# Kernel tuning notes

Hardware: AMD Instinct MI355X
Metric: run time of the kernel (lower is better)

Reference implementation:

```python
import jax, jax.numpy as jnp
import numpy as np

N, F, H, L, O, E = 20000, 128, 128, 4, 64, 640000
NEG_SLOPE = 0.2  # PyG GATConv default


def setup_inputs() -> dict:
    key = jax.random.key(0)
    ks = jax.random.split(key, 8)
    x = jax.random.normal(ks[0], (N, F), dtype=jnp.float32)
    edge_index = jax.random.randint(ks[1], (2, E), 0, N, dtype=jnp.int64)
    sc = 1.0 / np.sqrt(F)
    Ws = jax.random.normal(ks[2], (L, F, H), dtype=jnp.float32) * sc
    att_src = jax.random.normal(ks[3], (L, H), dtype=jnp.float32) * sc
    att_dst = jax.random.normal(ks[4], (L, H), dtype=jnp.float32) * sc
    biases = jnp.zeros((L, H), dtype=jnp.float32)
    W_out = jax.random.normal(ks[5], (H, O), dtype=jnp.float32) * (1.0 / np.sqrt(H))
    b_out = jnp.zeros((O,), dtype=jnp.float32)
    return {"x": x, "edge_index": edge_index, "Ws": Ws, "att_src": att_src,
            "att_dst": att_dst, "biases": biases, "W_out": W_out, "b_out": b_out}


def _gat_conv(h, src, dst, W, a_s, a_d, b):
    # h: [N, F_in]; single-head GATConv (PyG semantics)
    z = h @ W                                   # [N, H]
    alpha_s = z @ a_s                           # [N]
    alpha_d = z @ a_d                           # [N]
    logits = jax.nn.leaky_relu(alpha_s[src] + alpha_d[dst], negative_slope=NEG_SLOPE)  # [E']
    # segment-softmax over edges grouped by destination node
    m = jax.ops.segment_max(logits, dst, num_segments=N)
    p = jnp.exp(logits - m[dst])
    s = jax.ops.segment_sum(p, dst, num_segments=N)
    alpha = p / (s[dst] + 1e-16)                # [E']
    out = jax.ops.segment_sum(alpha[:, None] * z[src], dst, num_segments=N)  # [N, H]
    return out + b


def reference(x, edge_index, Ws, att_src, att_dst, biases, W_out, b_out):
    # add self-loops once (PyG GATConv default add_self_loops=True)
    loop = jnp.arange(N, dtype=edge_index.dtype)
    src = jnp.concatenate([edge_index[0], loop])
    dst = jnp.concatenate([edge_index[1], loop])
    h = x
    for l in range(L):
        h = _gat_conv(h, src, dst, Ws[l], att_src[l], att_dst[l], biases[l])
        h = jax.nn.relu(h)  # Dropout is identity at eval
    return h @ W_out + b_out  # [N, O]
```

## Files before the change

### kernel.cpp

```cpp
#include <hip/hip_runtime.h>

#define NN 20000
#define FF 128
#define HH 128
#define LL 4
#define OO 64
#define EE 640000
#define ET (EE + NN)
#define NEG 0.2f
#define NB ((NN + 255) / 256)
#define NTILES (NN / 16)

typedef short bf16x8 __attribute__((ext_vector_type(8)));
typedef float f32x4 __attribute__((ext_vector_type(4)));

__device__ inline ushort f2bf(float f) {
    uint u = __float_as_uint(f);
    return (ushort)((u + 0x7fffu + ((u >> 16) & 1u)) >> 16);
}


__global__ void k_init_counters(int* __restrict__ counters) {
    int i = blockIdx.x * 256 + threadIdx.x;
    if (i < NN) counters[i] = 1;
}

__global__ void k_hist(const int* __restrict__ dst, int* __restrict__ counters) {
    int e = blockIdx.x * 256 + threadIdx.x;
    if (e < EE) atomicAdd(&counters[dst[e]], 1);
}

__global__ void k_partial(const int* __restrict__ counters, int* __restrict__ partials) {
    __shared__ int ws[4];
    int t = threadIdx.x;
    int i = blockIdx.x * 256 + t;
    int c = (i < NN) ? counters[i] : 0;
    #pragma unroll
    for (int off = 32; off; off >>= 1) c += __shfl_xor(c, off);
    if ((t & 63) == 0) ws[t >> 6] = c;
    __syncthreads();
    if (t == 0) partials[blockIdx.x] = ws[0] + ws[1] + ws[2] + ws[3];
}

__global__ void k_scan_small(const int* __restrict__ partials, int* __restrict__ offsets) {
    __shared__ int sp[128];
    int t = threadIdx.x;
    int v = (t < NB) ? partials[t] : 0;
    sp[t] = v;
    __syncthreads();
    for (int off = 1; off < 128; off <<= 1) {
        int u = (t >= off) ? sp[t - off] : 0;
        __syncthreads();
        sp[t] += u;
        __syncthreads();
    }
    if (t < NB) offsets[t] = sp[t] - v;
}

__global__ void k_apply(const int* __restrict__ counters, const int* __restrict__ offsets,
                        int* __restrict__ row_off, int* __restrict__ cursor,
                        int2* __restrict__ edges) {
    __shared__ int sc[256];
    int t = threadIdx.x;
    int i = blockIdx.x * 256 + t;
    int c = (i < NN) ? counters[i] : 0;
    sc[t] = c;
    __syncthreads();
    for (int off = 1; off < 256; off <<= 1) {
        int u = (t >= off) ? sc[t - off] : 0;
        __syncthreads();
        sc[t] += u;
        __syncthreads();
    }
    int incl = sc[t];
    int base = offsets[blockIdx.x];
    if (i < NN) {
        int excl = base + incl - c;
        row_off[i] = excl;
        cursor[i] = excl + 1;
        edges[excl] = make_int2(i, i);
        if (i == NN - 1) row_off[NN] = base + incl;
    }
}

__global__ void k_scatter(const int* __restrict__ src, const int* __restrict__ dst,
                          int* __restrict__ cursor, int2* __restrict__ edges) {
    int e = blockIdx.x * 256 + threadIdx.x;
    if (e < EE) {
        int d = dst[e];
        int pidx = atomicAdd(&cursor[d], 1);
        edges[pidx] = make_int2(src[e], d);
    }
}


__global__ void k_convw(const float* __restrict__ Ws, const float* __restrict__ Wout,
                        ushort* __restrict__ wh, ushort* __restrict__ wl) {
    int idx = blockIdx.x * 256 + threadIdx.x;
    const int per_l = HH * 128;
    float v;
    if (idx < LL * per_l) {
        int l = idx / per_l, rem = idx % per_l;
        int n = rem >> 7, k = rem & 127;
        v = Ws[(size_t)l * 128 * HH + (size_t)k * HH + n];
    } else {
        int j = idx - LL * per_l;
        if (j >= OO * 128) return;
        int n = j >> 7, k = j & 127;
        v = Wout[(size_t)k * OO + n];
    }
    ushort h = f2bf(v);
    float hf = __uint_as_float((uint)h << 16);
    wh[idx] = h;
    wl[idx] = f2bf(v - hf);
}


__global__ void k_wa(const float* __restrict__ Ws, const float* __restrict__ attS,
                     const float* __restrict__ attD, float* __restrict__ wa) {
    int t = blockIdx.x * 256 + threadIdx.x;
    if (t >= LL * 256) return;
    int l = t >> 8, rem = t & 255, which = rem >> 7, k = rem & 127;
    const float* wrow = Ws + (size_t)l * 128 * HH + (size_t)k * HH;
    const float* av = (which ? attD : attS) + l * HH;
    float s = 0.f;
    #pragma unroll 4
    for (int n = 0; n < HH; n++) s += wrow[n] * av[n];
    wa[l * 256 + which * 128 + k] = s;
}


__global__ void k_ew(const float* __restrict__ asv, const float* __restrict__ adv,
                     const int2* __restrict__ edges, float2* __restrict__ pe) {
    int e = blockIdx.x * 256 + threadIdx.x;
    if (e >= ET) return;
    int2 ed = edges[e];
    float ad_ = adv[ed.y];
    float ls = asv[ed.x] + ad_;  ls = (ls >= 0.f) ? ls : NEG * ls;
    float ld = asv[ed.y] + ad_;  ld = (ld >= 0.f) ? ld : NEG * ld;
    float2 o;
    o.x = __expf(ls - ld);
    o.y = __int_as_float(ed.x);
    pe[e] = o;
}


__global__ __launch_bounds__(256)
void k_agg(const float* __restrict__ z, const float2* __restrict__ pe,
           const int* __restrict__ row_off, const float* __restrict__ bias,
           float* __restrict__ h) {
    int node = blockIdx.x * 4 + (threadIdx.x >> 6);
    int l64 = threadIdx.x & 63;
    if (node >= NN) return;
    int g = l64 >> 5, cl = l64 & 31;
    int beg = row_off[node], end = row_off[node + 1], lim = end - 1;
    const float4* zb = (const float4*)z;

    float4 acc = make_float4(0.f, 0.f, 0.f, 0.f);
    float s = 0.f;
    for (int e = beg + g * 8; e < end; e += 16) {
        int i1 = min(e + 1, lim), i2 = min(e + 2, lim), i3 = min(e + 3, lim);
        int i4 = min(e + 4, lim), i5 = min(e + 5, lim), i6 = min(e + 6, lim), i7 = min(e + 7, lim);
        float2 q0 = pe[e],  q1 = pe[i1], q2 = pe[i2], q3 = pe[i3];
        float2 q4 = pe[i4], q5 = pe[i5], q6 = pe[i6], q7 = pe[i7];
        int s0 = __float_as_int(q0.y), s1 = __float_as_int(q1.y);
        int s2 = __float_as_int(q2.y), s3 = __float_as_int(q3.y);
        int s4 = __float_as_int(q4.y), s5 = __float_as_int(q5.y);
        int s6 = __float_as_int(q6.y), s7 = __float_as_int(q7.y);
        float p0 = q0.x;
        float p1 = (e + 1 < end) ? q1.x : 0.f;
        float p2 = (e + 2 < end) ? q2.x : 0.f;
        float p3 = (e + 3 < end) ? q3.x : 0.f;
        float p4 = (e + 4 < end) ? q4.x : 0.f;
        float p5 = (e + 5 < end) ? q5.x : 0.f;
        float p6 = (e + 6 < end) ? q6.x : 0.f;
        float p7 = (e + 7 < end) ? q7.x : 0.f;
        float4 z0 = zb[(size_t)s0 * 32 + cl];
        float4 z1 = zb[(size_t)s1 * 32 + cl];
        float4 z2 = zb[(size_t)s2 * 32 + cl];
        float4 z3 = zb[(size_t)s3 * 32 + cl];
        float4 z4 = zb[(size_t)s4 * 32 + cl];
        float4 z5 = zb[(size_t)s5 * 32 + cl];
        float4 z6 = zb[(size_t)s6 * 32 + cl];
        float4 z7 = zb[(size_t)s7 * 32 + cl];
        s += ((p0 + p1) + (p2 + p3)) + ((p4 + p5) + (p6 + p7));
        acc.x += (p0 * z0.x + p1 * z1.x + p2 * z2.x + p3 * z3.x)
               + (p4 * z4.x + p5 * z5.x + p6 * z6.x + p7 * z7.x);
        acc.y += (p0 * z0.y + p1 * z1.y + p2 * z2.y + p3 * z3.y)
               + (p4 * z4.y + p5 * z5.y + p6 * z6.y + p7 * z7.y);
        acc.z += (p0 * z0.z + p1 * z1.z + p2 * z2.z + p3 * z3.z)
               + (p4 * z4.z + p5 * z5.z + p6 * z6.z + p7 * z7.z);
        acc.w += (p0 * z0.w + p1 * z1.w + p2 * z2.w + p3 * z3.w)
               + (p4 * z4.w + p5 * z5.w + p6 * z6.w + p7 * z7.w);
    }

    acc.x += __shfl_xor(acc.x, 32);
    acc.y += __shfl_xor(acc.y, 32);
    acc.z += __shfl_xor(acc.z, 32);
    acc.w += __shfl_xor(acc.w, 32);
    s     += __shfl_xor(s, 32);

    if (g == 0) {
        float inv = 1.f / (s + 1e-16f);
        float4 b = ((const float4*)bias)[cl];
        float4 o;
        o.x = fmaxf(acc.x * inv + b.x, 0.f);
        o.y = fmaxf(acc.y * inv + b.y, 0.f);
        o.z = fmaxf(acc.z * inv + b.z, 0.f);
        o.w = fmaxf(acc.w * inv + b.w, 0.f);
        ((float4*)h)[(size_t)node * 32 + cl] = o;
    }
}


template <int NCOL, bool BIAS, bool ALPHAS>
__global__ __launch_bounds__(256)
void k_gemm2(const float* __restrict__ A, const ushort* __restrict__ wh,
             const ushort* __restrict__ wl, const float* __restrict__ bias,
             float* __restrict__ C, const float* __restrict__ wa,
             float* __restrict__ as_o, float* __restrict__ ad_o) {
    __shared__ float h[16][132];
    int t = threadIdx.x;
    int row0 = blockIdx.x * 16;
    for (int i = t; i < 512; i += 256) {
        int r = i >> 5, c4 = (i & 31) << 2;
        *(float4*)&h[r][c4] = *(const float4*)&A[(size_t)(row0 + r) * 128 + c4];
    }
    __syncthreads();

    int wid = t >> 6, l64 = t & 63;
    constexpr int CT = NCOL / 32;
    if (wid >= CT) return;
    int lr = l64 & 15, lg = l64 >> 4;
    int col0 = wid * 32;

    f32x4 af0[4], af1[4];
    #pragma unroll
    for (int s = 0; s < 4; s++) {
        af0[s] = *(const f32x4*)&h[lr][s * 32 + lg * 8];
        af1[s] = *(const f32x4*)&h[lr][s * 32 + lg * 8 + 4];
    }
    bf16x8 ah[4], al[4];
    #pragma unroll
    for (int s = 0; s < 4; s++) {
        #pragma unroll
        for (int j = 0; j < 8; j++) {
            float v = (j < 4) ? af0[s][j] : af1[s][j - 4];
            ushort hb = f2bf(v);
            float hf = __uint_as_float((uint)hb << 16);
            ah[s][j] = (short)hb;
            al[s][j] = (short)f2bf(v - hf);
        }
    }

    f32x4 acc[2] = {{0.f, 0.f, 0.f, 0.f}, {0.f, 0.f, 0.f, 0.f}};
    #pragma unroll
    for (int s = 0; s < 4; s++) {
        #pragma unroll
        for (int nt = 0; nt < 2; nt++) {
            int woff = (col0 + nt * 16 + lr) * 128 + s * 32 + lg * 8;
            bf16x8 bh = *(const bf16x8*)(wh + woff);
            bf16x8 bl = *(const bf16x8*)(wl + woff);
            acc[nt] = __builtin_amdgcn_mfma_f32_16x16x32_bf16(ah[s], bh, acc[nt], 0, 0, 0);
            acc[nt] = __builtin_amdgcn_mfma_f32_16x16x32_bf16(ah[s], bl, acc[nt], 0, 0, 0);
            acc[nt] = __builtin_amdgcn_mfma_f32_16x16x32_bf16(al[s], bh, acc[nt], 0, 0, 0);
        }
    }

    int orow = lg * 4;
    #pragma unroll
    for (int nt = 0; nt < 2; nt++) {
        int c = col0 + nt * 16 + lr;
        #pragma unroll
        for (int r = 0; r < 4; r++) {
            float v = acc[nt][r];
            if (BIAS) v += bias[c];
            C[(size_t)(row0 + orow + r) * NCOL + c] = v;
        }
    }

    if constexpr (ALPHAS) {
        if (wid == 0) {
            float ps = 0.f, pd = 0.f;
            #pragma unroll
            for (int s = 0; s < 4; s++) {
                #pragma unroll
                for (int j = 0; j < 8; j++) {
                    float v = (j < 4) ? af0[s][j] : af1[s][j - 4];
                    int k = s * 32 + lg * 8 + j;
                    ps += v * wa[k];
                    pd += v * wa[128 + k];
                }
            }
            ps += __shfl_xor(ps, 16);  pd += __shfl_xor(pd, 16);
            ps += __shfl_xor(ps, 32);  pd += __shfl_xor(pd, 32);
            if (lg == 0) {
                as_o[row0 + lr] = ps;
                ad_o[row0 + lr] = pd;
            }
        }
    }
}


extern "C" void kernel_launch(void* const* d_in, const int* in_sizes, int n_in,
                              void* d_out, int out_size, void* d_ws, size_t ws_size,
                              hipStream_t stream) {
    const float* x      = (const float*)d_in[0];
    const int*   ei     = (const int*)d_in[1];
    const float* Ws     = (const float*)d_in[2];
    const float* attS   = (const float*)d_in[3];
    const float* attD   = (const float*)d_in[4];
    const float* biases = (const float*)d_in[5];
    const float* W_out  = (const float*)d_in[6];
    const float* b_out  = (const float*)d_in[7];
    float* out = (float*)d_out;

    const int* srcp = ei;
    const int* dstp = ei + EE;

    char* w = (char*)d_ws;
    auto take = [&](size_t bytes) {
        char* p = w;
        w += (bytes + 15) & ~(size_t)15;
        return p;
    };
    float*  za         = (float*)take((size_t)NN * HH * 4);
    float*  zbv        = (float*)take((size_t)NN * HH * 4);
    float*  hbuf       = (float*)take((size_t)NN * HH * 4);
    float*  asa        = (float*)take((size_t)NN * 4);
    float*  ada        = (float*)take((size_t)NN * 4);
    float*  asb        = (float*)take((size_t)NN * 4);
    float*  adb        = (float*)take((size_t)NN * 4);
    int*    counters   = (int*)take((size_t)NN * 4);
    int*    row_off    = (int*)take((size_t)(NN + 1) * 4);
    int*    cursor     = (int*)take((size_t)NN * 4);
    int2*   edges      = (int2*)take((size_t)ET * 8);
    float2* pebuf      = (float2*)take((size_t)ET * 8);
    int*    partials   = (int*)take((size_t)NB * 4);
    int*    offsets    = (int*)take((size_t)NB * 4);
    const int WTOT = LL * HH * 128 + OO * 128;
    ushort* whbuf      = (ushort*)take((size_t)WTOT * 2);
    ushort* wlbuf      = (ushort*)take((size_t)WTOT * 2);
    float*  wabuf      = (float*)take((size_t)LL * 256 * 4);

    k_init_counters<<<(NN + 255) / 256, 256, 0, stream>>>(counters);
    k_hist<<<(EE + 255) / 256, 256, 0, stream>>>(dstp, counters);
    k_partial<<<NB, 256, 0, stream>>>(counters, partials);
    k_scan_small<<<1, 128, 0, stream>>>(partials, offsets);
    k_apply<<<NB, 256, 0, stream>>>(counters, offsets, row_off, cursor, edges);
    k_scatter<<<(EE + 255) / 256, 256, 0, stream>>>(srcp, dstp, cursor, edges);
    k_convw<<<(WTOT + 255) / 256, 256, 0, stream>>>(Ws, W_out, whbuf, wlbuf);
    k_wa<<<(LL * 256 + 255) / 256, 256, 0, stream>>>(Ws, attS, attD, wabuf);

    const int agg_blocks = (NN + 3) / 4;
    const int ew_blocks  = (ET + 255) / 256;

    k_gemm2<HH, false, true><<<NTILES, 256, 0, stream>>>(
        x, whbuf, wlbuf, nullptr, za, wabuf, asa, ada);

    const float* zi[3]  = {za, zbv, za};
    float*       zo[3]  = {zbv, za, zbv};
    const float* asi[3] = {asa, asb, asa};
    const float* adi[3] = {ada, adb, ada};
    float*       aso[3] = {asb, asa, asb};
    float*       ado[3] = {adb, ada, adb};
    for (int l = 0; l < 3; l++) {
        k_ew<<<ew_blocks, 256, 0, stream>>>(asi[l], adi[l], edges, pebuf);
        k_agg<<<agg_blocks, 256, 0, stream>>>(zi[l], pebuf, row_off,
                                              biases + l * HH, hbuf);
        k_gemm2<HH, false, true><<<NTILES, 256, 0, stream>>>(
            hbuf, whbuf + (size_t)(l + 1) * HH * 128, wlbuf + (size_t)(l + 1) * HH * 128,
            nullptr, zo[l], wabuf + (l + 1) * 256, aso[l], ado[l]);
    }

    k_ew<<<ew_blocks, 256, 0, stream>>>(asb, adb, edges, pebuf);
    k_agg<<<agg_blocks, 256, 0, stream>>>(zbv, pebuf, row_off,
                                          biases + 3 * HH, hbuf);
    k_gemm2<OO, true, false><<<NTILES, 256, 0, stream>>>(
        hbuf, whbuf + (size_t)LL * HH * 128, wlbuf + (size_t)LL * HH * 128,
        b_out, out, nullptr, nullptr, nullptr);
}
```

Baseline: 321.6 us.

## Split aggregation into four column-slab passes over a slab-packed z layout

The GEMM now writes z in a packed layout of four 32-column slabs, each contiguous over all nodes ([4][N][32]). Aggregation becomes four launches, one per slab, with 8 lanes per edge covering 32 columns and 8 edges in flight per wave. The aim is to keep each pass's gathered working set (about 2.5 MB per slab) resident in cache so random source-row gathers hit L2 instead of HBM. The cost is reading the CSR and edge-weight arrays four times, four times as many launches, and fewer independent gathers per lane.

```diff
diff --git a/kernel.cpp b/kernel.cpp
--- a/kernel.cpp
+++ b/kernel.cpp
@@ -146,74 +146,56 @@
 
 
 __global__ __launch_bounds__(256)
-void k_agg(const float* __restrict__ z, const float2* __restrict__ pe,
-           const int* __restrict__ row_off, const float* __restrict__ bias,
-           float* __restrict__ h) {
+void k_aggq(const float* __restrict__ zq, const float2* __restrict__ pe,
+            const int* __restrict__ row_off, const float* __restrict__ bias,
+            float* __restrict__ h, int q) {
     int node = blockIdx.x * 4 + (threadIdx.x >> 6);
     int l64 = threadIdx.x & 63;
     if (node >= NN) return;
-    int g = l64 >> 5, cl = l64 & 31;
+    int c4 = l64 & 7, ep = l64 >> 3;
     int beg = row_off[node], end = row_off[node + 1], lim = end - 1;
-    const float4* zb = (const float4*)z;
+    const float* qb = zq + (size_t)q * NN * 32;
 
     float4 acc = make_float4(0.f, 0.f, 0.f, 0.f);
     float s = 0.f;
-    for (int e = beg + g * 8; e < end; e += 16) {
-        int i1 = min(e + 1, lim), i2 = min(e + 2, lim), i3 = min(e + 3, lim);
-        int i4 = min(e + 4, lim), i5 = min(e + 5, lim), i6 = min(e + 6, lim), i7 = min(e + 7, lim);
-        float2 q0 = pe[e],  q1 = pe[i1], q2 = pe[i2], q3 = pe[i3];
-        float2 q4 = pe[i4], q5 = pe[i5], q6 = pe[i6], q7 = pe[i7];
+    for (int e = beg + ep; e < end; e += 16) {
+        int i1 = min(e + 8, lim);
+        float2 q0 = pe[e], q1 = pe[i1];
         int s0 = __float_as_int(q0.y), s1 = __float_as_int(q1.y);
-        int s2 = __float_as_int(q2.y), s3 = __float_as_int(q3.y);
-        int s4 = __float_as_int(q4.y), s5 = __float_as_int(q5.y);
-        int s6 = __float_as_int(q6.y), s7 = __float_as_int(q7.y);
         float p0 = q0.x;
-        float p1 = (e + 1 < end) ? q1.x : 0.f;
-        float p2 = (e + 2 < end) ? q2.x : 0.f;
-        float p3 = (e + 3 < end) ? q3.x : 0.f;
-        float p4 = (e + 4 < end) ? q4.x : 0.f;
-        float p5 = (e + 5 < end) ? q5.x : 0.f;
-        float p6 = (e + 6 < end) ? q6.x : 0.f;
-        float p7 = (e + 7 < end) ? q7.x : 0.f;
-        float4 z0 = zb[(size_t)s0 * 32 + cl];
-        float4 z1 = zb[(size_t)s1 * 32 + cl];
-        float4 z2 = zb[(size_t)s2 * 32 + cl];
-        float4 z3 = zb[(size_t)s3 * 32 + cl];
-        float4 z4 = zb[(size_t)s4 * 32 + cl];
-        float4 z5 = zb[(size_t)s5 * 32 + cl];
-        float4 z6 = zb[(size_t)s6 * 32 + cl];
-        float4 z7 = zb[(size_t)s7 * 32 + cl];
-        s += ((p0 + p1) + (p2 + p3)) + ((p4 + p5) + (p6 + p7));
-        acc.x += (p0 * z0.x + p1 * z1.x + p2 * z2.x + p3 * z3.x)
-               + (p4 * z4.x + p5 * z5.x + p6 * z6.x + p7 * z7.x);
-        acc.y += (p0 * z0.y + p1 * z1.y + p2 * z2.y + p3 * z3.y)
-               + (p4 * z4.y + p5 * z5.y + p6 * z6.y + p7 * z7.y);
-        acc.z += (p0 * z0.z + p1 * z1.z + p2 * z2.z + p3 * z3.z)
-               + (p4 * z4.z + p5 * z5.z + p6 * z6.z + p7 * z7.z);
-        acc.w += (p0 * z0.w + p1 * z1.w + p2 * z2.w + p3 * z3.w)
-               + (p4 * z4.w + p5 * z5.w + p6 * z6.w + p7 * z7.w);
-    }
-
-    acc.x += __shfl_xor(acc.x, 32);
-    acc.y += __shfl_xor(acc.y, 32);
-    acc.z += __shfl_xor(acc.z, 32);
-    acc.w += __shfl_xor(acc.w, 32);
-    s     += __shfl_xor(s, 32);
-
-    if (g == 0) {
+        float p1 = (e + 8 < end) ? q1.x : 0.f;
+        float4 z0 = *(const float4*)(qb + (size_t)s0 * 32 + c4 * 4);
+        float4 z1 = *(const float4*)(qb + (size_t)s1 * 32 + c4 * 4);
+        s += p0 + p1;
+        acc.x += p0 * z0.x + p1 * z1.x;
+        acc.y += p0 * z0.y + p1 * z1.y;
+        acc.z += p0 * z0.z + p1 * z1.z;
+        acc.w += p0 * z0.w + p1 * z1.w;
+    }
+
+    #pragma unroll
+    for (int off = 8; off < 64; off <<= 1) {
+        acc.x += __shfl_xor(acc.x, off);
+        acc.y += __shfl_xor(acc.y, off);
+        acc.z += __shfl_xor(acc.z, off);
+        acc.w += __shfl_xor(acc.w, off);
+        s     += __shfl_xor(s, off);
+    }
+
+    if (ep == 0) {
         float inv = 1.f / (s + 1e-16f);
-        float4 b = ((const float4*)bias)[cl];
+        float4 b = *(const float4*)(bias + q * 32 + c4 * 4);
         float4 o;
         o.x = fmaxf(acc.x * inv + b.x, 0.f);
         o.y = fmaxf(acc.y * inv + b.y, 0.f);
         o.z = fmaxf(acc.z * inv + b.z, 0.f);
         o.w = fmaxf(acc.w * inv + b.w, 0.f);
-        ((float4*)h)[(size_t)node * 32 + cl] = o;
-    }
-}
-
-
-template <int NCOL, bool BIAS, bool ALPHAS>
+        *(float4*)&h[(size_t)node * 128 + q * 32 + c4 * 4] = o;
+    }
+}
+
+
+template <int NCOL, bool BIAS, bool ALPHAS, bool PACKED>
 __global__ __launch_bounds__(256)
 void k_gemm2(const float* __restrict__ A, const ushort* __restrict__ wh,
              const ushort* __restrict__ wl, const float* __restrict__ bias,
@@ -275,7 +257,10 @@
         for (int r = 0; r < 4; r++) {
             float v = acc[nt][r];
             if (BIAS) v += bias[c];
-            C[(size_t)(row0 + orow + r) * NCOL + c] = v;
+            if (PACKED)
+                C[((size_t)(c >> 5) * NN + (row0 + orow + r)) * 32 + (c & 31)] = v;
+            else
+                C[(size_t)(row0 + orow + r) * NCOL + c] = v;
         }
     }
 
@@ -356,7 +341,7 @@
     const int agg_blocks = (NN + 3) / 4;
     const int ew_blocks  = (ET + 255) / 256;
 
-    k_gemm2<HH, false, true><<<NTILES, 256, 0, stream>>>(
+    k_gemm2<HH, false, true, true><<<NTILES, 256, 0, stream>>>(
         x, whbuf, wlbuf, nullptr, za, wabuf, asa, ada);
 
     const float* zi[3]  = {za, zbv, za};
@@ -367,17 +352,19 @@
     float*       ado[3] = {adb, ada, adb};
     for (int l = 0; l < 3; l++) {
         k_ew<<<ew_blocks, 256, 0, stream>>>(asi[l], adi[l], edges, pebuf);
-        k_agg<<<agg_blocks, 256, 0, stream>>>(zi[l], pebuf, row_off,
-                                              biases + l * HH, hbuf);
-        k_gemm2<HH, false, true><<<NTILES, 256, 0, stream>>>(
+        for (int q = 0; q < 4; q++)
+            k_aggq<<<agg_blocks, 256, 0, stream>>>(zi[l], pebuf, row_off,
+                                                   biases + l * HH, hbuf, q);
+        k_gemm2<HH, false, true, true><<<NTILES, 256, 0, stream>>>(
             hbuf, whbuf + (size_t)(l + 1) * HH * 128, wlbuf + (size_t)(l + 1) * HH * 128,
             nullptr, zo[l], wabuf + (l + 1) * 256, aso[l], ado[l]);
     }
 
     k_ew<<<ew_blocks, 256, 0, stream>>>(asb, adb, edges, pebuf);
-    k_agg<<<agg_blocks, 256, 0, stream>>>(zbv, pebuf, row_off,
-                                          biases + 3 * HH, hbuf);
-    k_gemm2<OO, true, false><<<NTILES, 256, 0, stream>>>(
+    for (int q = 0; q < 4; q++)
+        k_aggq<<<agg_blocks, 256, 0, stream>>>(zbv, pebuf, row_off,
+                                               biases + 3 * HH, hbuf, q);
+    k_gemm2<OO, true, false, false><<<NTILES, 256, 0, stream>>>(
         hbuf, whbuf + (size_t)LL * HH * 128, wlbuf + (size_t)LL * HH * 128,
         b_out, out, nullptr, nullptr, nullptr);
 }
```

After: 370.6 us. 15.3% more time.

## Fuse edge-weight computation into aggregation kernel and memset counters

Applied to the files above, without the earlier changes.

The per-edge logit and exp computation moves from a separate k_ew kernel, which wrote a float2 buffer, into k_agg. k_agg now reads the source index from the edge list, gathers asv[src], and computes leaky-relu and exp relative to the self-loop logit. This removes four kernel launches and the write and read of a 5 MB intermediate per layer. The cost is redundant exp work in each lane and an extra scattered gather of asv in the hot loop. Counter init is also replaced with hipMemsetAsync to zero plus +1 added at read time.

```diff
diff --git a/kernel.cpp b/kernel.cpp
--- a/kernel.cpp
+++ b/kernel.cpp
@@ -20,11 +20,6 @@
 }
 
 
-__global__ void k_init_counters(int* __restrict__ counters) {
-    int i = blockIdx.x * 256 + threadIdx.x;
-    if (i < NN) counters[i] = 1;
-}
-
 __global__ void k_hist(const int* __restrict__ dst, int* __restrict__ counters) {
     int e = blockIdx.x * 256 + threadIdx.x;
     if (e < EE) atomicAdd(&counters[dst[e]], 1);
@@ -34,7 +29,7 @@
     __shared__ int ws[4];
     int t = threadIdx.x;
     int i = blockIdx.x * 256 + t;
-    int c = (i < NN) ? counters[i] : 0;
+    int c = (i < NN) ? counters[i] + 1 : 0;
     #pragma unroll
     for (int off = 32; off; off >>= 1) c += __shfl_xor(c, off);
     if ((t & 63) == 0) ws[t >> 6] = c;
@@ -63,7 +58,7 @@
     __shared__ int sc[256];
     int t = threadIdx.x;
     int i = blockIdx.x * 256 + t;
-    int c = (i < NN) ? counters[i] : 0;
+    int c = (i < NN) ? counters[i] + 1 : 0;
     sc[t] = c;
     __syncthreads();
     for (int off = 1; off < 256; off <<= 1) {
@@ -130,30 +125,19 @@
 }
 
 
-__global__ void k_ew(const float* __restrict__ asv, const float* __restrict__ adv,
-                     const int2* __restrict__ edges, float2* __restrict__ pe) {
-    int e = blockIdx.x * 256 + threadIdx.x;
-    if (e >= ET) return;
-    int2 ed = edges[e];
-    float ad_ = adv[ed.y];
-    float ls = asv[ed.x] + ad_;  ls = (ls >= 0.f) ? ls : NEG * ls;
-    float ld = asv[ed.y] + ad_;  ld = (ld >= 0.f) ? ld : NEG * ld;
-    float2 o;
-    o.x = __expf(ls - ld);
-    o.y = __int_as_float(ed.x);
-    pe[e] = o;
-}
-
-
 __global__ __launch_bounds__(256)
-void k_agg(const float* __restrict__ z, const float2* __restrict__ pe,
-           const int* __restrict__ row_off, const float* __restrict__ bias,
+void k_agg(const float* __restrict__ z, const int2* __restrict__ edges,
+           const int* __restrict__ row_off, const float* __restrict__ asv,
+           const float* __restrict__ adv, const float* __restrict__ bias,
            float* __restrict__ h) {
     int node = blockIdx.x * 4 + (threadIdx.x >> 6);
     int l64 = threadIdx.x & 63;
     if (node >= NN) return;
     int g = l64 >> 5, cl = l64 & 31;
     int beg = row_off[node], end = row_off[node + 1], lim = end - 1;
+    float adn = adv[node];
+    float lself = asv[node] + adn;
+    float mx = (lself >= 0.f) ? lself : NEG * lself;
     const float4* zb = (const float4*)z;
 
     float4 acc = make_float4(0.f, 0.f, 0.f, 0.f);
@@ -161,20 +145,14 @@
     for (int e = beg + g * 8; e < end; e += 16) {
         int i1 = min(e + 1, lim), i2 = min(e + 2, lim), i3 = min(e + 3, lim);
         int i4 = min(e + 4, lim), i5 = min(e + 5, lim), i6 = min(e + 6, lim), i7 = min(e + 7, lim);
-        float2 q0 = pe[e],  q1 = pe[i1], q2 = pe[i2], q3 = pe[i3];
-        float2 q4 = pe[i4], q5 = pe[i5], q6 = pe[i6], q7 = pe[i7];
-        int s0 = __float_as_int(q0.y), s1 = __float_as_int(q1.y);
-        int s2 = __float_as_int(q2.y), s3 = __float_as_int(q3.y);
-        int s4 = __float_as_int(q4.y), s5 = __float_as_int(q5.y);
-        int s6 = __float_as_int(q6.y), s7 = __float_as_int(q7.y);
-        float p0 = q0.x;
-        float p1 = (e + 1 < end) ? q1.x : 0.f;
-        float p2 = (e + 2 < end) ? q2.x : 0.f;
-        float p3 = (e + 3 < end) ? q3.x : 0.f;
-        float p4 = (e + 4 < end) ? q4.x : 0.f;
-        float p5 = (e + 5 < end) ? q5.x : 0.f;
-        float p6 = (e + 6 < end) ? q6.x : 0.f;
-        float p7 = (e + 7 < end) ? q7.x : 0.f;
+        int s0 = edges[e].x,  s1 = edges[i1].x, s2 = edges[i2].x, s3 = edges[i3].x;
+        int s4 = edges[i4].x, s5 = edges[i5].x, s6 = edges[i6].x, s7 = edges[i7].x;
+        float l0 = asv[s0] + adn, l1 = asv[s1] + adn, l2 = asv[s2] + adn, l3 = asv[s3] + adn;
+        float l4 = asv[s4] + adn, l5 = asv[s5] + adn, l6 = asv[s6] + adn, l7 = asv[s7] + adn;
+        l0 = (l0 >= 0.f) ? l0 : NEG * l0;  l1 = (l1 >= 0.f) ? l1 : NEG * l1;
+        l2 = (l2 >= 0.f) ? l2 : NEG * l2;  l3 = (l3 >= 0.f) ? l3 : NEG * l3;
+        l4 = (l4 >= 0.f) ? l4 : NEG * l4;  l5 = (l5 >= 0.f) ? l5 : NEG * l5;
+        l6 = (l6 >= 0.f) ? l6 : NEG * l6;  l7 = (l7 >= 0.f) ? l7 : NEG * l7;
         float4 z0 = zb[(size_t)s0 * 32 + cl];
         float4 z1 = zb[(size_t)s1 * 32 + cl];
         float4 z2 = zb[(size_t)s2 * 32 + cl];
@@ -183,6 +161,14 @@
         float4 z5 = zb[(size_t)s5 * 32 + cl];
         float4 z6 = zb[(size_t)s6 * 32 + cl];
         float4 z7 = zb[(size_t)s7 * 32 + cl];
+        float p0 = __expf(l0 - mx);
+        float p1 = (e + 1 < end) ? __expf(l1 - mx) : 0.f;
+        float p2 = (e + 2 < end) ? __expf(l2 - mx) : 0.f;
+        float p3 = (e + 3 < end) ? __expf(l3 - mx) : 0.f;
+        float p4 = (e + 4 < end) ? __expf(l4 - mx) : 0.f;
+        float p5 = (e + 5 < end) ? __expf(l5 - mx) : 0.f;
+        float p6 = (e + 6 < end) ? __expf(l6 - mx) : 0.f;
+        float p7 = (e + 7 < end) ? __expf(l7 - mx) : 0.f;
         s += ((p0 + p1) + (p2 + p3)) + ((p4 + p5) + (p6 + p7));
         acc.x += (p0 * z0.x + p1 * z1.x + p2 * z2.x + p3 * z3.x)
                + (p4 * z4.x + p5 * z5.x + p6 * z6.x + p7 * z7.x);
@@ -336,7 +322,6 @@
     int*    row_off    = (int*)take((size_t)(NN + 1) * 4);
     int*    cursor     = (int*)take((size_t)NN * 4);
     int2*   edges      = (int2*)take((size_t)ET * 8);
-    float2* pebuf      = (float2*)take((size_t)ET * 8);
     int*    partials   = (int*)take((size_t)NB * 4);
     int*    offsets    = (int*)take((size_t)NB * 4);
     const int WTOT = LL * HH * 128 + OO * 128;
@@ -344,7 +329,7 @@
     ushort* wlbuf      = (ushort*)take((size_t)WTOT * 2);
     float*  wabuf      = (float*)take((size_t)LL * 256 * 4);
 
-    k_init_counters<<<(NN + 255) / 256, 256, 0, stream>>>(counters);
+    hipMemsetAsync(counters, 0, (size_t)NN * 4, stream);
     k_hist<<<(EE + 255) / 256, 256, 0, stream>>>(dstp, counters);
     k_partial<<<NB, 256, 0, stream>>>(counters, partials);
     k_scan_small<<<1, 128, 0, stream>>>(partials, offsets);
@@ -354,7 +339,6 @@
     k_wa<<<(LL * 256 + 255) / 256, 256, 0, stream>>>(Ws, attS, attD, wabuf);
 
     const int agg_blocks = (NN + 3) / 4;
-    const int ew_blocks  = (ET + 255) / 256;
 
     k_gemm2<HH, false, true><<<NTILES, 256, 0, stream>>>(
         x, whbuf, wlbuf, nullptr, za, wabuf, asa, ada);
@@ -366,16 +350,14 @@
     float*       aso[3] = {asb, asa, asb};
     float*       ado[3] = {adb, ada, adb};
     for (int l = 0; l < 3; l++) {
-        k_ew<<<ew_blocks, 256, 0, stream>>>(asi[l], adi[l], edges, pebuf);
-        k_agg<<<agg_blocks, 256, 0, stream>>>(zi[l], pebuf, row_off,
+        k_agg<<<agg_blocks, 256, 0, stream>>>(zi[l], edges, row_off, asi[l], adi[l],
                                               biases + l * HH, hbuf);
         k_gemm2<HH, false, true><<<NTILES, 256, 0, stream>>>(
             hbuf, whbuf + (size_t)(l + 1) * HH * 128, wlbuf + (size_t)(l + 1) * HH * 128,
             nullptr, zo[l], wabuf + (l + 1) * 256, aso[l], ado[l]);
     }
 
-    k_ew<<<ew_blocks, 256, 0, stream>>>(asb, adb, edges, pebuf);
-    k_agg<<<agg_blocks, 256, 0, stream>>>(zbv, pebuf, row_off,
+    k_agg<<<agg_blocks, 256, 0, stream>>>(zbv, edges, row_off, asb, adb,
                                           biases + 3 * HH, hbuf);
     k_gemm2<OO, true, false><<<NTILES, 256, 0, stream>>>(
         hbuf, whbuf + (size_t)LL * HH * 128, wlbuf + (size_t)LL * HH * 128,
```

New measurement: 314.0 us. 2.4% less time.
